# Kernel optimization log

Measured on AMD Instinct MI355X. Metric: run time of the kernel, lower is better.

The kernel has to match this reference:

```python
import jax, jax.numpy as jnp
import numpy as np

B, C, N = 16, 1024, 32
H, Dh = 8, 16          # num_head, dim per head
D = H * Dh             # 128, model feature dim
SCALE = 0.5


def setup_inputs() -> dict:
    key = jax.random.key(0)
    ks = jax.random.split(key, 12)
    inp = {
        "atom_query": jax.random.normal(ks[0], (B, C, D), jnp.float32),
        "atom_neighbor": jax.random.normal(ks[1], (B, C, N, D), jnp.float32),
        "local_distance": jax.random.uniform(ks[2], (B, C, N, 1), jnp.float32),
        "mask": jnp.ones((B, C, N), jnp.float32),
        # Dense params (kernel [in, out], bias [out]) as in keras Dense
        "Wq": jax.random.normal(ks[3], (D, D), jnp.float32) / np.sqrt(D),
        "bq": jnp.zeros((D,), jnp.float32),
        "Wk": jax.random.normal(ks[4], (D, D), jnp.float32) / np.sqrt(D),
        "bk": jnp.zeros((D,), jnp.float32),
        "Wv": jax.random.normal(ks[5], (D, D), jnp.float32) / np.sqrt(D),
        "bv": jnp.zeros((D,), jnp.float32),
        "Wf": jax.random.normal(ks[6], (1, D), jnp.float32),
        "bf": jnp.zeros((D,), jnp.float32),
    }
    return inp


def reference(atom_query, atom_neighbor, local_distance, mask,
              Wq, bq, Wk, bk, Wv, bv, Wf, bf):
    # distance filter with swish activation: x * sigmoid(x)
    ld = local_distance @ Wf + bf              # [B,C,N,D]
    ld = ld * jax.nn.sigmoid(ld)
    an = atom_neighbor * ld                    # distance-gated neighbors

    query = atom_query @ Wq + bq               # [B,C,D]
    k = (an @ Wk + bk).reshape(B, C, N, H, Dh)  # [B,C,N,H,d]
    v = (an @ Wv + bv).reshape(B, C, N, H, Dh)

    q = query.reshape(B, C, H, Dh) * (float(Dh) ** (-SCALE))
    energy = jnp.einsum('bchd,bcnhd->bhcn', q, k)           # [B,H,C,N]
    energy = energy + (1.0 - mask[:, None, :, :]) * (-1e9)
    attn = jax.nn.softmax(energy, axis=-1)

    ctx = jnp.einsum('bhcn,bcnhd->bcnhd', attn, v)          # per-neighbor context
    ctx = ctx * mask[:, :, :, None, None]
    ctx = ctx.reshape(B, C, N, H * Dh)
    context = jnp.sum(ctx, axis=2) + query                  # [B,C,D]
    return attn, context
```

## Files before the change

kernel.cpp:

```cpp
#include <hip/hip_runtime.h>
#include <hip/hip_bf16.h>
#include <cstdint>


#define B_ 16
#define C_ 1024
#define N_ 32
#define H_ 8
#define D_ 128
#define G_ 4
#define T_ 256

typedef unsigned short u16;
typedef unsigned int u32;

__device__ __forceinline__ float bflo(u32 u) {
    union { u32 i; float f; } v; v.i = u << 16; return v.f;
}
__device__ __forceinline__ float bfhi(u32 u) {
    union { u32 i; float f; } v; v.i = u & 0xffff0000u; return v.f;
}
__device__ __forceinline__ u16 f2bf(float f) {
    union { float f; u32 i; } v; v.f = f;
    u32 x = v.i;
    u32 r = (x + 0x7fffu + ((x >> 16) & 1u)) >> 16;
    return (u16)r;
}
__device__ __forceinline__ u32 pack2(float a, float b) {
    return (u32)f2bf(a) | ((u32)f2bf(b) << 16);
}
__device__ __forceinline__ float swishf(float x) {
    float s = __builtin_amdgcn_rcpf(1.0f + __expf(-x));
    return x * s;
}

__global__ __launch_bounds__(T_, 2)
void la_kernel(const float* __restrict__ aq_g,  const float* __restrict__ an_g,
               const float* __restrict__ dist_g, const float* __restrict__ mask_g,
               const float* __restrict__ wq_g,  const float* __restrict__ bq_g,
               const float* __restrict__ wk_g,
               const float* __restrict__ wv_g,  const float* __restrict__ bv_g,
               const float* __restrict__ wf_g,  const float* __restrict__ bfb_g,
               float* __restrict__ attn_o, float* __restrict__ ctx_o)
{
    __shared__ __align__(16) u16   s_an[G_ * N_ * 136];
    __shared__ __align__(16) float s_ts[G_ * H_ * 132];
    __shared__ float s_q[G_][D_];
    __shared__ float s_aq[G_][D_];
    __shared__ float s_eat[G_][H_][33];
    __shared__ float s_ao[G_][H_][N_];
    __shared__ float s_dist[G_][N_];
    __shared__ float s_mask[G_][N_];
    __shared__ float s_asum[G_][H_];
    __shared__ __align__(16) float s_wf[D_];
    __shared__ __align__(16) float s_bfb[D_];

    const int tid = threadIdx.x;
    const int b   = blockIdx.x >> 8;
    const int c0  = (blockIdx.x & 255) << 2;

    const int op = tid & 63;
    const int js = tid >> 6;

    float2 wq2[32];
    #pragma unroll
    for (int i = 0; i < 32; i++)
        wq2[i] = ((const float2*)(wq_g + (size_t)(js * 32 + i) * D_))[op];

    if (tid < D_) {
        s_wf[tid]  = wf_g[tid];
        s_bfb[tid] = bfb_g[tid];
        int c = tid >> 5, n = tid & 31;
        int gi = (b * C_ + c0 + c) * N_ + n;
        s_dist[c][n] = dist_g[gi];
        s_mask[c][n] = mask_g[gi];
    }
    {
        int c = tid >> 7, d = tid & 127;
        s_aq[c][d] = aq_g[(b * C_ + c0 + c) * D_ + d];
        int i2 = tid + 256;
        c = i2 >> 7; d = i2 & 127;
        s_aq[c][d] = aq_g[(b * C_ + c0 + c) * D_ + d];
    }
    __syncthreads();

    {
        const float4* gan = (const float4*)(an_g + (size_t)(b * C_ + c0) * N_ * D_);
        #pragma unroll
        for (int k = 0; k < 16; k++) {
            int ci = k * T_ + tid;
            float4 v = gan[ci];
            int d4 = ci & 31, n = (ci >> 5) & 31, c = ci >> 10;
            float dist = s_dist[c][n];
            int d0 = d4 << 2;
            float4 wf = *(const float4*)&s_wf[d0];
            float4 bb = *(const float4*)&s_bfb[d0];
            float g0 = swishf(fmaf(dist, wf.x, bb.x));
            float g1 = swishf(fmaf(dist, wf.y, bb.y));
            float g2 = swishf(fmaf(dist, wf.z, bb.z));
            float g3 = swishf(fmaf(dist, wf.w, bb.w));
            u32 o0 = pack2(v.x * g0, v.y * g1);
            u32 o1 = pack2(v.z * g2, v.w * g3);
            *(uint2*)(s_an + (c * N_ + n) * 136 + d0) = make_uint2(o0, o1);
        }
    }

    {
        float acc0[G_], acc1[G_];
        #pragma unroll
        for (int c = 0; c < G_; c++) { acc0[c] = 0.f; acc1[c] = 0.f; }
        #pragma unroll
        for (int i4 = 0; i4 < 8; i4++) {
            #pragma unroll
            for (int c = 0; c < G_; c++) {
                float4 a4 = *(const float4*)&s_aq[c][js * 32 + i4 * 4];
                float2 w0 = wq2[i4 * 4], w1 = wq2[i4 * 4 + 1];
                float2 w2 = wq2[i4 * 4 + 2], w3 = wq2[i4 * 4 + 3];
                acc0[c] = fmaf(a4.x, w0.x, acc0[c]); acc1[c] = fmaf(a4.x, w0.y, acc1[c]);
                acc0[c] = fmaf(a4.y, w1.x, acc0[c]); acc1[c] = fmaf(a4.y, w1.y, acc1[c]);
                acc0[c] = fmaf(a4.z, w2.x, acc0[c]); acc1[c] = fmaf(a4.z, w2.y, acc1[c]);
                acc0[c] = fmaf(a4.w, w3.x, acc0[c]); acc1[c] = fmaf(a4.w, w3.y, acc1[c]);
            }
        }
        float* s_part = s_ts;
        #pragma unroll
        for (int c = 0; c < G_; c++) {
            *(float2*)&s_part[(js * G_ + c) * D_ + 2 * op] = make_float2(acc0[c], acc1[c]);
        }
    }
    __syncthreads();

    {
        const float* s_part = s_ts;
        #pragma unroll
        for (int r = 0; r < 2; r++) {
            int lin = r * 256 + tid;
            int c = lin >> 7, od = lin & 127;
            float sum = s_part[(0 * G_ + c) * D_ + od] + s_part[(1 * G_ + c) * D_ + od]
                      + s_part[(2 * G_ + c) * D_ + od] + s_part[(3 * G_ + c) * D_ + od];
            s_q[c][od] = sum + bq_g[od];
        }
    }
    __syncthreads();

    float2 wv2[32];
    #pragma unroll
    for (int i = 0; i < 32; i++)
        wv2[i] = ((const float2*)(wv_g + (size_t)(js * 32 + i) * D_))[op];

    {
        int h = tid & 7, jb = tid >> 3;
        float wk[4][16];
        #pragma unroll
        for (int jj = 0; jj < 4; jj++) {
            int j = jb + jj * 32;
            const float4* pk = (const float4*)(wk_g + j * D_ + h * 16);
            float4 k0 = pk[0], k1 = pk[1], k2 = pk[2], k3 = pk[3];
            wk[jj][0]  = k0.x; wk[jj][1]  = k0.y; wk[jj][2]  = k0.z; wk[jj][3]  = k0.w;
            wk[jj][4]  = k1.x; wk[jj][5]  = k1.y; wk[jj][6]  = k1.z; wk[jj][7]  = k1.w;
            wk[jj][8]  = k2.x; wk[jj][9]  = k2.y; wk[jj][10] = k2.z; wk[jj][11] = k2.w;
            wk[jj][12] = k3.x; wk[jj][13] = k3.y; wk[jj][14] = k3.z; wk[jj][15] = k3.w;
        }
        #pragma unroll
        for (int c = 0; c < G_; c++) {
            float qv[16];
            #pragma unroll
            for (int d = 0; d < 16; d++) qv[d] = s_q[c][h * 16 + d];
            #pragma unroll
            for (int jj = 0; jj < 4; jj++) {
                float acc = 0.f;
                #pragma unroll
                for (int d = 0; d < 16; d++) acc = fmaf(qv[d], wk[jj][d], acc);
                s_ts[(c * H_ + h) * 132 + jb + jj * 32] = acc * 0.25f;
            }
        }
    }
    __syncthreads();

    {
        int c = tid >> 6, h = (tid >> 3) & 7, n0 = tid & 7;
        const float* trow = &s_ts[(c * H_ + h) * 132];
        float acc[4] = {0.f, 0.f, 0.f, 0.f};
        #pragma unroll
        for (int jc = 0; jc < 16; jc++) {
            float4 ta = *(const float4*)(trow + jc * 8);
            float4 tb = *(const float4*)(trow + jc * 8 + 4);
            #pragma unroll
            for (int r = 0; r < 4; r++) {
                int n = n0 + r * 8;
                uint4 av = *(const uint4*)(s_an + (c * N_ + n) * 136 + jc * 8);
                float s = acc[r];
                s = fmaf(bflo(av.x), ta.x, s);  s = fmaf(bfhi(av.x), ta.y, s);
                s = fmaf(bflo(av.y), ta.z, s);  s = fmaf(bfhi(av.y), ta.w, s);
                s = fmaf(bflo(av.z), tb.x, s);  s = fmaf(bfhi(av.z), tb.y, s);
                s = fmaf(bflo(av.w), tb.z, s);  s = fmaf(bfhi(av.w), tb.w, s);
                acc[r] = s;
            }
        }
        #pragma unroll
        for (int r = 0; r < 4; r++) {
            int n = n0 + r * 8;
            float mk = s_mask[c][n];
            s_eat[c][h][n] = acc[r] + (1.0f - mk) * (-1.0e9f);
        }
    }
    __syncthreads();

    if (tid < G_ * H_) {
        int c = tid >> 3, h = tid & 7;
        float e[N_];
        float m = -3.0e38f;
        #pragma unroll
        for (int n = 0; n < N_; n++) { e[n] = s_eat[c][h][n]; m = fmaxf(m, e[n]); }
        float sum = 0.f;
        #pragma unroll
        for (int n = 0; n < N_; n++) { float p = __expf(e[n] - m); e[n] = p; sum += p; }
        float inv = 1.0f / sum;
        float asum = 0.f;
        #pragma unroll
        for (int n = 0; n < N_; n++) {
            float a  = e[n] * inv;
            float am = a * s_mask[c][n];
            s_ao[c][h][n]  = a;
            s_eat[c][h][n] = am;
            asum += am;
        }
        s_asum[c][h] = asum;
    }
    __syncthreads();

    {
        int ch = tid >> 3, i8 = tid & 7;
        int c = ch >> 3, h = ch & 7;
        float4 w;
        w.x = s_ao[c][h][i8 * 4];
        w.y = s_ao[c][h][i8 * 4 + 1];
        w.z = s_ao[c][h][i8 * 4 + 2];
        w.w = s_ao[c][h][i8 * 4 + 3];
        size_t off = ((size_t)(b * H_ + h) * C_ + (c0 + c)) * N_ + i8 * 4;
        *(float4*)(attn_o + off) = w;
    }

    {
        int c = tid >> 6, h = (tid >> 3) & 7, jg = tid & 7;
        int j0 = jg * 16;
        float acc[16];
        #pragma unroll
        for (int i = 0; i < 16; i++) acc[i] = 0.f;
        #pragma unroll 4
        for (int n = 0; n < N_; n++) {
            float am = s_eat[c][h][n];
            const u16* arow = s_an + (c * N_ + n) * 136 + j0;
            uint4 v0 = *(const uint4*)(arow);
            uint4 v1 = *(const uint4*)(arow + 8);
            acc[0]  = fmaf(am, bflo(v0.x), acc[0]);   acc[1]  = fmaf(am, bfhi(v0.x), acc[1]);
            acc[2]  = fmaf(am, bflo(v0.y), acc[2]);   acc[3]  = fmaf(am, bfhi(v0.y), acc[3]);
            acc[4]  = fmaf(am, bflo(v0.z), acc[4]);   acc[5]  = fmaf(am, bfhi(v0.z), acc[5]);
            acc[6]  = fmaf(am, bflo(v0.w), acc[6]);   acc[7]  = fmaf(am, bfhi(v0.w), acc[7]);
            acc[8]  = fmaf(am, bflo(v1.x), acc[8]);   acc[9]  = fmaf(am, bfhi(v1.x), acc[9]);
            acc[10] = fmaf(am, bflo(v1.y), acc[10]);  acc[11] = fmaf(am, bfhi(v1.y), acc[11]);
            acc[12] = fmaf(am, bflo(v1.z), acc[12]);  acc[13] = fmaf(am, bfhi(v1.z), acc[13]);
            acc[14] = fmaf(am, bflo(v1.w), acc[14]);  acc[15] = fmaf(am, bfhi(v1.w), acc[15]);
        }
        float* srow = &s_ts[(c * H_ + h) * 132 + j0];
        *(float4*)(srow)      = make_float4(acc[0], acc[1], acc[2], acc[3]);
        *(float4*)(srow + 4)  = make_float4(acc[4], acc[5], acc[6], acc[7]);
        *(float4*)(srow + 8)  = make_float4(acc[8], acc[9], acc[10], acc[11]);
        *(float4*)(srow + 12) = make_float4(acc[12], acc[13], acc[14], acc[15]);
    }
    __syncthreads();

    {
        int h = op >> 3;
        float acc0[G_], acc1[G_];
        #pragma unroll
        for (int c = 0; c < G_; c++) { acc0[c] = 0.f; acc1[c] = 0.f; }
        #pragma unroll
        for (int i4 = 0; i4 < 8; i4++) {
            #pragma unroll
            for (int c = 0; c < G_; c++) {
                float4 s4 = *(const float4*)&s_ts[(c * H_ + h) * 132 + js * 32 + i4 * 4];
                float2 w0 = wv2[i4 * 4], w1 = wv2[i4 * 4 + 1];
                float2 w2 = wv2[i4 * 4 + 2], w3 = wv2[i4 * 4 + 3];
                acc0[c] = fmaf(s4.x, w0.x, acc0[c]); acc1[c] = fmaf(s4.x, w0.y, acc1[c]);
                acc0[c] = fmaf(s4.y, w1.x, acc0[c]); acc1[c] = fmaf(s4.y, w1.y, acc1[c]);
                acc0[c] = fmaf(s4.z, w2.x, acc0[c]); acc1[c] = fmaf(s4.z, w2.y, acc1[c]);
                acc0[c] = fmaf(s4.w, w3.x, acc0[c]); acc1[c] = fmaf(s4.w, w3.y, acc1[c]);
            }
        }
        float* s_gp = (float*)s_an;
        #pragma unroll
        for (int c = 0; c < G_; c++) {
            *(float2*)&s_gp[(js * G_ + c) * D_ + 2 * op] = make_float2(acc0[c], acc1[c]);
        }
    }
    __syncthreads();

    {
        const float* s_gp = (const float*)s_an;
        #pragma unroll
        for (int r = 0; r < 2; r++) {
            int lin = r * 256 + tid;
            int c = lin >> 7, od = lin & 127;
            int h = od >> 4;
            float sum = s_gp[(0 * G_ + c) * D_ + od] + s_gp[(1 * G_ + c) * D_ + od]
                      + s_gp[(2 * G_ + c) * D_ + od] + s_gp[(3 * G_ + c) * D_ + od];
            float r0 = sum + s_asum[c][h] * bv_g[od] + s_q[c][od];
            ctx_o[((size_t)(b * C_ + c0 + c)) * D_ + od] = r0;
        }
    }
}

extern "C" void kernel_launch(void* const* d_in, const int* in_sizes, int n_in,
                              void* d_out, int out_size, void* d_ws, size_t ws_size,
                              hipStream_t stream) {
    const float* aq   = (const float*)d_in[0];
    const float* an   = (const float*)d_in[1];
    const float* dist = (const float*)d_in[2];
    const float* mask = (const float*)d_in[3];
    const float* wq   = (const float*)d_in[4];
    const float* bq   = (const float*)d_in[5];
    const float* wk   = (const float*)d_in[6];
    const float* wv   = (const float*)d_in[8];
    const float* bv   = (const float*)d_in[9];
    const float* wf   = (const float*)d_in[10];
    const float* bfb  = (const float*)d_in[11];

    float* attn_o = (float*)d_out;
    float* ctx_o  = attn_o + (size_t)B_ * H_ * C_ * N_;

    dim3 grid(B_ * C_ / G_), block(T_);
    hipLaunchKernelGGL(la_kernel, grid, block, 0, stream,
                       aq, an, dist, mask, wq, bq, wk, wv, bv, wf, bfb,
                       attn_o, ctx_o);
}
```

Measured before the change: 461.9 us.

## Switch gated neighbors to fp16 and use packed dot2/hfma2 math

Stores gated neighbor features as fp16 (converted with the pkrtz instruction) in place of software-rounded bf16. The energy loop now uses packed fp16 dot2 with a pre-packed fp16 query-key row, and the context accumulation uses packed half2 FMAs. The attention store is folded into the softmax thread, which removes the s_ao buffer and one pass over it. The aim is fewer conversion and FMA instructions, at the cost of fp16 range and rounding risk, especially from accumulating the context in half precision over 32 neighbors.

```diff
diff --git a/kernel.cpp b/kernel.cpp
--- a/kernel.cpp
+++ b/kernel.cpp
@@ -1,5 +1,5 @@
 #include <hip/hip_runtime.h>
-#include <hip/hip_bf16.h>
+#include <hip/hip_fp16.h>
 #include <cstdint>
 
 
@@ -13,21 +13,25 @@
 
 typedef unsigned short u16;
 typedef unsigned int u32;
-
-__device__ __forceinline__ float bflo(u32 u) {
-    union { u32 i; float f; } v; v.i = u << 16; return v.f;
-}
-__device__ __forceinline__ float bfhi(u32 u) {
-    union { u32 i; float f; } v; v.i = u & 0xffff0000u; return v.f;
-}
-__device__ __forceinline__ u16 f2bf(float f) {
-    union { float f; u32 i; } v; v.f = f;
-    u32 x = v.i;
-    u32 r = (x + 0x7fffu + ((x >> 16) & 1u)) >> 16;
-    return (u16)r;
-}
-__device__ __forceinline__ u32 pack2(float a, float b) {
-    return (u32)f2bf(a) | ((u32)f2bf(b) << 16);
+typedef __fp16 hw2 __attribute__((ext_vector_type(2)));
+
+__device__ __forceinline__ u32 pkrtz(float a, float b) {
+    hw2 r = __builtin_amdgcn_cvt_pkrtz(a, b);
+    return __builtin_bit_cast(u32, r);
+}
+__device__ __forceinline__ float fdot2(u32 a, u32 b, float c) {
+#if __has_builtin(__builtin_amdgcn_fdot2)
+    return __builtin_amdgcn_fdot2(__builtin_bit_cast(hw2, a),
+                                  __builtin_bit_cast(hw2, b), c, false);
+#else
+    float2 A = __half22float2(__builtin_bit_cast(__half2, a));
+    float2 B = __half22float2(__builtin_bit_cast(__half2, b));
+    return fmaf(A.y, B.y, fmaf(A.x, B.x, c));
+#endif
+}
+__device__ __forceinline__ __half2 fma2(u32 a, u32 b, __half2 c) {
+    return __hfma2(__builtin_bit_cast(__half2, a),
+                   __builtin_bit_cast(__half2, b), c);
 }
 __device__ __forceinline__ float swishf(float x) {
     float s = __builtin_amdgcn_rcpf(1.0f + __expf(-x));
@@ -47,8 +51,7 @@
     __shared__ __align__(16) float s_ts[G_ * H_ * 132];
     __shared__ float s_q[G_][D_];
     __shared__ float s_aq[G_][D_];
-    __shared__ float s_eat[G_][H_][33];
-    __shared__ float s_ao[G_][H_][N_];
+    __shared__ __align__(8) float s_eat[G_][H_][33];
     __shared__ float s_dist[G_][N_];
     __shared__ float s_mask[G_][N_];
     __shared__ float s_asum[G_][H_];
@@ -99,8 +102,8 @@
             float g1 = swishf(fmaf(dist, wf.y, bb.y));
             float g2 = swishf(fmaf(dist, wf.z, bb.z));
             float g3 = swishf(fmaf(dist, wf.w, bb.w));
-            u32 o0 = pack2(v.x * g0, v.y * g1);
-            u32 o1 = pack2(v.z * g2, v.w * g3);
+            u32 o0 = pkrtz(v.x * g0, v.y * g1);
+            u32 o1 = pkrtz(v.z * g2, v.w * g3);
             *(uint2*)(s_an + (c * N_ + n) * 136 + d0) = make_uint2(o0, o1);
         }
     }
@@ -149,11 +152,12 @@
         wv2[i] = ((const float2*)(wv_g + (size_t)(js * 32 + i) * D_))[op];
 
     {
+        u32* t32 = (u32*)s_ts;
         int h = tid & 7, jb = tid >> 3;
         float wk[4][16];
         #pragma unroll
         for (int jj = 0; jj < 4; jj++) {
-            int j = jb + jj * 32;
+            int j = 2 * jb + (jj & 1) + (jj >> 1) * 64;
             const float4* pk = (const float4*)(wk_g + j * D_ + h * 16);
             float4 k0 = pk[0], k1 = pk[1], k2 = pk[2], k3 = pk[3];
             wk[jj][0]  = k0.x; wk[jj][1]  = k0.y; wk[jj][2]  = k0.z; wk[jj][3]  = k0.w;
@@ -166,34 +170,37 @@
             float qv[16];
             #pragma unroll
             for (int d = 0; d < 16; d++) qv[d] = s_q[c][h * 16 + d];
+            float acc[4];
             #pragma unroll
             for (int jj = 0; jj < 4; jj++) {
-                float acc = 0.f;
+                float a = 0.f;
                 #pragma unroll
-                for (int d = 0; d < 16; d++) acc = fmaf(qv[d], wk[jj][d], acc);
-                s_ts[(c * H_ + h) * 132 + jb + jj * 32] = acc * 0.25f;
+                for (int d = 0; d < 16; d++) a = fmaf(qv[d], wk[jj][d], a);
+                acc[jj] = a * 0.25f;
             }
-        }
-    }
-    __syncthreads();
-
-    {
+            t32[(c * 8 + h) * 68 + jb]      = pkrtz(acc[0], acc[1]);
+            t32[(c * 8 + h) * 68 + 32 + jb] = pkrtz(acc[2], acc[3]);
+        }
+    }
+    __syncthreads();
+
+    {
+        const u32* t32 = (const u32*)s_ts;
         int c = tid >> 6, h = (tid >> 3) & 7, n0 = tid & 7;
-        const float* trow = &s_ts[(c * H_ + h) * 132];
+        const uint4* trow = (const uint4*)(t32 + (c * 8 + h) * 68);
         float acc[4] = {0.f, 0.f, 0.f, 0.f};
         #pragma unroll
         for (int jc = 0; jc < 16; jc++) {
-            float4 ta = *(const float4*)(trow + jc * 8);
-            float4 tb = *(const float4*)(trow + jc * 8 + 4);
+            uint4 t4 = trow[jc];
             #pragma unroll
             for (int r = 0; r < 4; r++) {
                 int n = n0 + r * 8;
-                uint4 av = *(const uint4*)(s_an + (c * N_ + n) * 136 + jc * 8);
+                uint4 a4 = *(const uint4*)(s_an + (c * N_ + n) * 136 + jc * 8);
                 float s = acc[r];
-                s = fmaf(bflo(av.x), ta.x, s);  s = fmaf(bfhi(av.x), ta.y, s);
-                s = fmaf(bflo(av.y), ta.z, s);  s = fmaf(bfhi(av.y), ta.w, s);
-                s = fmaf(bflo(av.z), tb.x, s);  s = fmaf(bfhi(av.z), tb.y, s);
-                s = fmaf(bflo(av.w), tb.z, s);  s = fmaf(bfhi(av.w), tb.w, s);
+                s = fdot2(a4.x, t4.x, s);
+                s = fdot2(a4.y, t4.y, s);
+                s = fdot2(a4.z, t4.z, s);
+                s = fdot2(a4.w, t4.w, s);
                 acc[r] = s;
             }
         }
@@ -216,57 +223,58 @@
         #pragma unroll
         for (int n = 0; n < N_; n++) { float p = __expf(e[n] - m); e[n] = p; sum += p; }
         float inv = 1.0f / sum;
+        u32* ampk = (u32*)&s_eat[c][h][0];
         float asum = 0.f;
-        #pragma unroll
-        for (int n = 0; n < N_; n++) {
-            float a  = e[n] * inv;
-            float am = a * s_mask[c][n];
-            s_ao[c][h][n]  = a;
-            s_eat[c][h][n] = am;
-            asum += am;
+        size_t off = ((size_t)(b * H_ + h) * C_ + (c0 + c)) * N_;
+        #pragma unroll
+        for (int n4 = 0; n4 < 8; n4++) {
+            float4 w;
+            w.x = e[n4 * 4]     * inv;
+            w.y = e[n4 * 4 + 1] * inv;
+            w.z = e[n4 * 4 + 2] * inv;
+            w.w = e[n4 * 4 + 3] * inv;
+            *(float4*)(attn_o + off + n4 * 4) = w;
+            float am0 = w.x * s_mask[c][n4 * 4];
+            float am1 = w.y * s_mask[c][n4 * 4 + 1];
+            float am2 = w.z * s_mask[c][n4 * 4 + 2];
+            float am3 = w.w * s_mask[c][n4 * 4 + 3];
+            asum += am0 + am1 + am2 + am3;
+            ampk[n4 * 4]     = pkrtz(am0, am0);
+            ampk[n4 * 4 + 1] = pkrtz(am1, am1);
+            ampk[n4 * 4 + 2] = pkrtz(am2, am2);
+            ampk[n4 * 4 + 3] = pkrtz(am3, am3);
         }
         s_asum[c][h] = asum;
     }
     __syncthreads();
 
     {
-        int ch = tid >> 3, i8 = tid & 7;
-        int c = ch >> 3, h = ch & 7;
-        float4 w;
-        w.x = s_ao[c][h][i8 * 4];
-        w.y = s_ao[c][h][i8 * 4 + 1];
-        w.z = s_ao[c][h][i8 * 4 + 2];
-        w.w = s_ao[c][h][i8 * 4 + 3];
-        size_t off = ((size_t)(b * H_ + h) * C_ + (c0 + c)) * N_ + i8 * 4;
-        *(float4*)(attn_o + off) = w;
-    }
-
-    {
         int c = tid >> 6, h = (tid >> 3) & 7, jg = tid & 7;
-        int j0 = jg * 16;
-        float acc[16];
-        #pragma unroll
-        for (int i = 0; i < 16; i++) acc[i] = 0.f;
+        const u32* ampk = (const u32*)&s_eat[c][h][0];
+        __half2 acc2[8];
+        #pragma unroll
+        for (int i = 0; i < 8; i++) acc2[i] = __float2half2_rn(0.f);
         #pragma unroll 4
         for (int n = 0; n < N_; n++) {
-            float am = s_eat[c][h][n];
-            const u16* arow = s_an + (c * N_ + n) * 136 + j0;
-            uint4 v0 = *(const uint4*)(arow);
-            uint4 v1 = *(const uint4*)(arow + 8);
-            acc[0]  = fmaf(am, bflo(v0.x), acc[0]);   acc[1]  = fmaf(am, bfhi(v0.x), acc[1]);
-            acc[2]  = fmaf(am, bflo(v0.y), acc[2]);   acc[3]  = fmaf(am, bfhi(v0.y), acc[3]);
-            acc[4]  = fmaf(am, bflo(v0.z), acc[4]);   acc[5]  = fmaf(am, bfhi(v0.z), acc[5]);
-            acc[6]  = fmaf(am, bflo(v0.w), acc[6]);   acc[7]  = fmaf(am, bfhi(v0.w), acc[7]);
-            acc[8]  = fmaf(am, bflo(v1.x), acc[8]);   acc[9]  = fmaf(am, bfhi(v1.x), acc[9]);
-            acc[10] = fmaf(am, bflo(v1.y), acc[10]);  acc[11] = fmaf(am, bfhi(v1.y), acc[11]);
-            acc[12] = fmaf(am, bflo(v1.z), acc[12]);  acc[13] = fmaf(am, bfhi(v1.z), acc[13]);
-            acc[14] = fmaf(am, bflo(v1.w), acc[14]);  acc[15] = fmaf(am, bfhi(v1.w), acc[15]);
-        }
-        float* srow = &s_ts[(c * H_ + h) * 132 + j0];
-        *(float4*)(srow)      = make_float4(acc[0], acc[1], acc[2], acc[3]);
-        *(float4*)(srow + 4)  = make_float4(acc[4], acc[5], acc[6], acc[7]);
-        *(float4*)(srow + 8)  = make_float4(acc[8], acc[9], acc[10], acc[11]);
-        *(float4*)(srow + 12) = make_float4(acc[12], acc[13], acc[14], acc[15]);
+            u32 am2 = ampk[n];
+            const uint4* arow = (const uint4*)(s_an + (c * N_ + n) * 136 + jg * 16);
+            uint4 a0 = arow[0], a1 = arow[1];
+            acc2[0] = fma2(a0.x, am2, acc2[0]);
+            acc2[1] = fma2(a0.y, am2, acc2[1]);
+            acc2[2] = fma2(a0.z, am2, acc2[2]);
+            acc2[3] = fma2(a0.w, am2, acc2[3]);
+            acc2[4] = fma2(a1.x, am2, acc2[4]);
+            acc2[5] = fma2(a1.y, am2, acc2[5]);
+            acc2[6] = fma2(a1.z, am2, acc2[6]);
+            acc2[7] = fma2(a1.w, am2, acc2[7]);
+        }
+        float* srow = &s_ts[(c * H_ + h) * 132 + jg * 16];
+        #pragma unroll
+        for (int p = 0; p < 4; p++) {
+            float2 lo = __half22float2(acc2[p * 2]);
+            float2 hi = __half22float2(acc2[p * 2 + 1]);
+            *(float4*)(srow + p * 4) = make_float4(lo.x, lo.y, hi.x, hi.y);
+        }
     }
     __syncthreads();
 
```

Measured after the change: 437.1 us. -5.4%, faster.
